# Performance work log

Measured on AMD Instinct MI355X. Metric: run time of the kernel, lower is better.

Reference implementation:

```python
import jax, jax.numpy as jnp
import numpy as np

B, T, C, FFN, N_LAYER, LAYER_ID = 4, 2048, 1024, 4096, 24, 1
EPS = 1e-5


def setup_inputs() -> dict:
    key = jax.random.key(0)
    ks = jax.random.split(key, 10)
    scale = 0.02

    def w(k, shape):
        return (jax.random.normal(k, shape, jnp.float32) * scale)

    # RWKV-4 init formulas for layer_id=1, n_layer=24 (learned params, init per source)
    r01 = LAYER_ID / (N_LAYER - 1)
    r10 = 1.0 - LAYER_ID / N_LAYER
    ddd = np.arange(C, dtype=np.float64) / C
    h = np.arange(C, dtype=np.float64)
    decay = -5.0 + 8.0 * (h / (C - 1)) ** (0.7 + 1.3 * r01)
    zigzag = np.array([(i + 1) % 3 - 1 for i in range(C)], dtype=np.float64) * 0.5
    tfirst = np.log(0.3) + zigzag

    return {
        "x": jax.random.normal(ks[0], (B, T, C), jnp.float32),
        "ln1_w": jnp.ones((C,), jnp.float32), "ln1_b": jnp.zeros((C,), jnp.float32),
        "ln2_w": jnp.ones((C,), jnp.float32), "ln2_b": jnp.zeros((C,), jnp.float32),
        "time_decay": jnp.asarray(decay, jnp.float32),
        "time_first": jnp.asarray(tfirst, jnp.float32),
        "tmk": jnp.asarray(ddd ** r10, jnp.float32),
        "tmv": jnp.asarray(ddd ** r10 + 0.3 * r01, jnp.float32),
        "tmr": jnp.asarray(ddd ** (0.5 * r10), jnp.float32),
        "att_kw": w(ks[1], (C, C)), "att_vw": w(ks[2], (C, C)),
        "att_rw": w(ks[3], (C, C)), "att_ow": w(ks[4], (C, C)),
        "f_tmk": jnp.asarray(ddd ** r10, jnp.float32),
        "f_tmr": jnp.asarray(ddd ** r10, jnp.float32),
        "f_kw": w(ks[5], (FFN, C)), "f_rw": w(ks[6], (C, C)), "f_vw": w(ks[7], (C, FFN)),
    }


def _ln(z, g, b):
    m = jnp.mean(z, axis=-1, keepdims=True)
    v = jnp.mean(jnp.square(z - m), axis=-1, keepdims=True)
    return (z - m) * jax.lax.rsqrt(v + EPS) * g + b


def _shift(z):  # token shift: prepend zero row along T, drop last
    return jnp.pad(z, ((0, 0), (1, 0), (0, 0)))[:, :-1]


def _wkv(time_decay, u, k, v):
    # Numerically-stable RWKV-4 WKV recurrence (log-space max trick).
    # k, v: [B, T, C]; time_decay, u: [C]
    w = -jnp.exp(time_decay)  # per-channel decay (negative)
    kt = jnp.moveaxis(k, 1, 0)  # [T, B, C]
    vt = jnp.moveaxis(v, 1, 0)
    aa = jnp.zeros_like(kt[0])
    bb = jnp.zeros_like(kt[0])
    pp = jnp.full_like(kt[0], -1e38)

    def step(carry, kv):
        aa, bb, pp = carry
        kk, vv = kv
        ww = u + kk
        p = jnp.maximum(pp, ww)
        e1 = jnp.exp(pp - p)
        e2 = jnp.exp(ww - p)
        out = (e1 * aa + e2 * vv) / (e1 * bb + e2)
        ww2 = pp + w
        p2 = jnp.maximum(ww2, kk)
        e1b = jnp.exp(ww2 - p2)
        e2b = jnp.exp(kk - p2)
        return (e1b * aa + e2b * vv, e1b * bb + e2b, p2), out

    _, out = jax.lax.scan(step, (aa, bb, pp), (kt, vt))
    return jnp.moveaxis(out, 0, 1)  # [B, T, C]


def reference(x, ln1_w, ln1_b, ln2_w, ln2_b, time_decay, time_first,
              tmk, tmv, tmr, att_kw, att_vw, att_rw, att_ow,
              f_tmk, f_tmr, f_kw, f_rw, f_vw):
    # --- RWKV_TimeMix (layer_id != 0; protectors are identity in fwd for finite vals) ---
    h = _ln(x, ln1_w, ln1_b)
    hx = _shift(h)
    xk = h * tmk + hx * (1.0 - tmk)
    xv = h * tmv + hx * (1.0 - tmv)
    xr = h * tmr + hx * (1.0 - tmr)
    k = jnp.einsum('btc,dc->btd', xk, att_kw)
    v = jnp.einsum('btc,dc->btd', xv, att_vw)
    sr = jax.nn.sigmoid(jnp.einsum('btc,dc->btd', xr, att_rw))
    rwkv = sr * _wkv(time_decay, time_first, k, v)
    x = x + jnp.einsum('btd,cd->btc', rwkv, att_ow)
    # --- RWKV_ChannelMix ---
    h = _ln(x, ln2_w, ln2_b)
    hx = _shift(h)
    xk = h * f_tmk + hx * (1.0 - f_tmk)
    xr = h * f_tmr + hx * (1.0 - f_tmr)
    kk = jnp.square(jax.nn.relu(jnp.einsum('btc,fc->btf', xk, f_kw)))
    kv = jnp.einsum('btf,cf->btc', kk, f_vw)
    x = x + jax.nn.sigmoid(jnp.einsum('btc,dc->btd', xr, f_rw)) * kv
    return x
```

## Files before the change

kernel.cpp:

```cpp
#include <hip/hip_runtime.h>
#include <cstdint>

#define C_DIM 1024
#define T_DIM 2048
#define B_DIM 4
#define FFN_DIM 4096
#define NROWS (B_DIM * T_DIM)
#define NELEM ((size_t)NROWS * C_DIM)
#define MB ((size_t)1 << 20)
#define NSEG 32
#define SEGL (T_DIM / NSEG)

typedef __bf16 bf16;
typedef __bf16 bf16x4 __attribute__((ext_vector_type(4)));
typedef __bf16 bf16x8 __attribute__((ext_vector_type(8)));
typedef float  floatx4 __attribute__((ext_vector_type(4)));

#define GLDS(g, l) __builtin_amdgcn_global_load_lds(                          \
    (const __attribute__((address_space(1))) void*)(g),                       \
    (__attribute__((address_space(3))) void*)(l), 16, 0, 0)

struct W7 {
    const float* s[7];
    bf16*        d[7];
    int          cum[8];
};

__global__ __launch_bounds__(256) void f2b7_kernel(W7 w)
{
    int id = blockIdx.x * 256 + threadIdx.x;
    int seg = 0;
#pragma unroll
    for (int j = 1; j < 7; ++j) if (id >= w.cum[j]) seg = j;
    int i = id - w.cum[seg];
    float4 v = ((const float4*)w.s[seg])[i];
    bf16x4 o = { (bf16)v.x, (bf16)v.y, (bf16)v.z, (bf16)v.w };
    ((bf16x4*)w.d[seg])[i] = o;
}

template<bool HASV>
__global__ __launch_bounds__(256) void lnmix_kernel(const float* __restrict__ x,
                                                    const float* __restrict__ g,
                                                    const float* __restrict__ b,
                                                    const float* __restrict__ mk,
                                                    const float* __restrict__ mv,
                                                    const float* __restrict__ mr,
                                                    bf16* __restrict__ xk,
                                                    bf16* __restrict__ xv,
                                                    bf16* __restrict__ xr)
{
    int row = blockIdx.x;
    int t   = row & (T_DIM - 1);
    int tid = threadIdx.x;
    size_t i4 = (size_t)row * 256 + tid;

    float4 v  = ((const float4*)x)[i4];
    float4 vp = make_float4(0.f, 0.f, 0.f, 0.f);
    if (t != 0) vp = ((const float4*)x)[i4 - 256];

    float s   = v.x + v.y + v.z + v.w;
    float s2  = v.x * v.x + v.y * v.y + v.z * v.z + v.w * v.w;
    float sp  = vp.x + vp.y + vp.z + vp.w;
    float sp2 = vp.x * vp.x + vp.y * vp.y + vp.z * vp.z + vp.w * vp.w;
    for (int off = 32; off > 0; off >>= 1) {
        s   += __shfl_down(s,   off);
        s2  += __shfl_down(s2,  off);
        sp  += __shfl_down(sp,  off);
        sp2 += __shfl_down(sp2, off);
    }
    __shared__ float red[16];
    int lane = tid & 63, wid = tid >> 6;
    if (lane == 0) { red[wid] = s; red[4 + wid] = s2; red[8 + wid] = sp; red[12 + wid] = sp2; }
    __syncthreads();
    s   = red[0] + red[1] + red[2] + red[3];
    s2  = red[4] + red[5] + red[6] + red[7];
    sp  = red[8] + red[9] + red[10] + red[11];
    sp2 = red[12] + red[13] + red[14] + red[15];

    float mean  = s * (1.0f / C_DIM);
    float inv   = rsqrtf(s2 * (1.0f / C_DIM) - mean * mean + 1e-5f);
    float meanp = sp * (1.0f / C_DIM);
    float invp  = rsqrtf(sp2 * (1.0f / C_DIM) - meanp * meanp + 1e-5f);

    float4 gv = ((const float4*)g)[tid];
    float4 bv = ((const float4*)b)[tid];
    float4 hv, hp;
    hv.x = (v.x - mean) * inv * gv.x + bv.x;
    hv.y = (v.y - mean) * inv * gv.y + bv.y;
    hv.z = (v.z - mean) * inv * gv.z + bv.z;
    hv.w = (v.w - mean) * inv * gv.w + bv.w;
    if (t != 0) {
        hp.x = (vp.x - meanp) * invp * gv.x + bv.x;
        hp.y = (vp.y - meanp) * invp * gv.y + bv.y;
        hp.z = (vp.z - meanp) * invp * gv.z + bv.z;
        hp.w = (vp.w - meanp) * invp * gv.w + bv.w;
    } else {
        hp = make_float4(0.f, 0.f, 0.f, 0.f);
    }

    float4 m1 = ((const float4*)mk)[tid];
    bf16x4 o;
    o.x = (bf16)(hp.x + m1.x * (hv.x - hp.x));
    o.y = (bf16)(hp.y + m1.y * (hv.y - hp.y));
    o.z = (bf16)(hp.z + m1.z * (hv.z - hp.z));
    o.w = (bf16)(hp.w + m1.w * (hv.w - hp.w));
    ((bf16x4*)xk)[i4] = o;

    if (HASV) {
        float4 m2 = ((const float4*)mv)[tid];
        o.x = (bf16)(hp.x + m2.x * (hv.x - hp.x));
        o.y = (bf16)(hp.y + m2.y * (hv.y - hp.y));
        o.z = (bf16)(hp.z + m2.z * (hv.z - hp.z));
        o.w = (bf16)(hp.w + m2.w * (hv.w - hp.w));
        ((bf16x4*)xv)[i4] = o;
    }

    float4 m3 = ((const float4*)mr)[tid];
    o.x = (bf16)(hp.x + m3.x * (hv.x - hp.x));
    o.y = (bf16)(hp.y + m3.y * (hv.y - hp.y));
    o.z = (bf16)(hp.z + m3.z * (hv.z - hp.z));
    o.w = (bf16)(hp.w + m3.w * (hv.w - hp.w));
    ((bf16x4*)xr)[i4] = o;
}

#define EPI_NONE 0
#define EPI_SIG 1
#define EPI_RELU2 2
#define EPI_ADD 3
#define EPI_SCALEADD 4

struct GemmArgs {
    const bf16* A;
    const bf16* W;
    void*       Y;
    const float* X2;
    const bf16*  S;
    int N, K, epi, outBf16;
};

__global__ __launch_bounds__(512) void gemm_p(GemmArgs pr)
{
    __shared__ unsigned short As[3 * 16384];
    __shared__ unsigned short Bs[3 * 8192];

    int tid = threadIdx.x;
    int lid = blockIdx.x;
    const bf16* PA = pr.A;
    const bf16* PW = pr.W;
    void*       PY = pr.Y;
    const float* PX2 = pr.X2;
    const bf16*  PS  = pr.S;
    int N = pr.N, K = pr.K;
    int epi = pr.epi, obf = pr.outBf16;

    int ntn = N >> 7;
    int m_t, n_t;
    if (ntn == 8) {
        int xcd = lid & 7, s = lid >> 3;
        n_t = s & 7;
        m_t = (xcd << 2) | (s >> 3);
    } else {
        int sq = lid >> 3;
        n_t = (lid & 7) * 4 + (sq & 3);
        m_t = sq >> 2;
    }
    int m0 = m_t * 256, n0 = n_t * 128;

    int wv = tid >> 6;
    int ln = tid & 63;

    int srow = wv * 16 + (ln >> 2);
    int qsw  = ((ln & 3) - ((srow >> 1) & 3)) & 3;
    const bf16* Ag = PA + (size_t)(m0 + srow) * K + qsw * 8;
    const bf16* Wg = PW + (size_t)(n0 + srow) * K + qsw * 8;
    size_t rowK128 = (size_t)128 * K;

    unsigned short* AsW = As + wv * 512;
    unsigned short* BsW = Bs + wv * 512;

    int wm = (wv & 3) * 64, wn = (wv >> 2) * 64;
    int ra0 = wm + (ln & 15);
    int rb0 = wn + (ln & 15);
    int qa  = ln >> 4;
    int abase = ra0 * 32 + (((qa + ((ra0 >> 1) & 3)) & 3) * 8);
    int bbase = rb0 * 32 + (((qa + ((rb0 >> 1) & 3)) & 3) * 8);

    floatx4 acc[4][4] = {};

#define STAGE_A(kt, bi)                                                       \
    do {                                                                      \
        const bf16* _a = Ag + (size_t)(kt) * 64;                              \
        unsigned short* _d = AsW + (bi) * 16384;                              \
        GLDS(_a,                _d);                                          \
        GLDS(_a + rowK128,      _d + 4096);                                   \
        GLDS(_a + 32,           _d + 8192);                                   \
        GLDS(_a + rowK128 + 32, _d + 12288);                                  \
    } while (0)
#define STAGE_B(kt, bi)                                                       \
    do {                                                                      \
        const bf16* _b = Wg + (size_t)(kt) * 64;                              \
        unsigned short* _d = BsW + (bi) * 8192;                               \
        GLDS(_b,      _d);                                                    \
        GLDS(_b + 32, _d + 4096);                                             \
    } while (0)

#define MFMA16(a, b)                                                          \
    do {                                                                      \
        _Pragma("unroll")                                                     \
        for (int i = 0; i < 4; ++i)                                           \
            _Pragma("unroll")                                                 \
            for (int j = 0; j < 4; ++j)                                       \
                acc[i][j] = __builtin_amdgcn_mfma_f32_16x16x32_bf16(          \
                    a[i], b[j], acc[i][j], 0, 0, 0);                          \
    } while (0)

    int nt = K >> 6;

    STAGE_A(0, 0); STAGE_B(0, 0);
    STAGE_A(1, 1); STAGE_B(1, 1);

    int bi = 0, bi2 = 2;
    for (int t = 0; t < nt; ++t) {
        if (t < nt - 1) asm volatile("s_waitcnt vmcnt(6)" ::: "memory");
        else            asm volatile("s_waitcnt vmcnt(0)" ::: "memory");
        __builtin_amdgcn_s_barrier();
        __builtin_amdgcn_sched_barrier(0);

        const unsigned short* A0 = As + bi * 16384 + abase;
        const unsigned short* B0 = Bs + bi * 8192  + bbase;
        int dost = (t + 2 < nt);

        bf16x8 a[4], b[4];
#pragma unroll
        for (int i = 0; i < 4; ++i) a[i] = *(const bf16x8*)(A0 + i * 512);
#pragma unroll
        for (int j = 0; j < 4; ++j) b[j] = *(const bf16x8*)(B0 + j * 512);
        if (dost) STAGE_A(t + 2, bi2);
        asm volatile("s_waitcnt lgkmcnt(0)" ::: "memory");
        __builtin_amdgcn_sched_barrier(0);
        MFMA16(a, b);

#pragma unroll
        for (int i = 0; i < 4; ++i) a[i] = *(const bf16x8*)(A0 + 8192 + i * 512);
#pragma unroll
        for (int j = 0; j < 4; ++j) b[j] = *(const bf16x8*)(B0 + 4096 + j * 512);
        if (dost) STAGE_B(t + 2, bi2);
        asm volatile("s_waitcnt lgkmcnt(0)" ::: "memory");
        __builtin_amdgcn_sched_barrier(0);
        MFMA16(a, b);

        bi  = (bi  == 2) ? 0 : bi  + 1;
        bi2 = (bi2 == 2) ? 0 : bi2 + 1;
    }

#undef STAGE_A
#undef STAGE_B
#undef MFMA16

    int row0 = (ln >> 4) * 4;
    int colb = n0 + wn + (ln & 15);
#pragma unroll
    for (int i = 0; i < 4; ++i) {
        int gm = m0 + wm + i * 16 + row0;
#pragma unroll
        for (int j = 0; j < 4; ++j) {
            int gn = colb + j * 16;
#pragma unroll
            for (int r = 0; r < 4; ++r) {
                size_t idx = (size_t)(gm + r) * N + gn;
                float v = acc[i][j][r];
                if (epi == EPI_SIG)        v = 1.0f / (1.0f + __expf(-v));
                else if (epi == EPI_RELU2) { float t2 = fmaxf(v, 0.0f); v = t2 * t2; }
                else if (epi == EPI_ADD)   v = PX2[idx] + v;
                else if (epi == EPI_SCALEADD) v = PX2[idx] + (float)PS[idx] * v;
                if (obf) ((bf16*)PY)[idx] = (bf16)v;
                else     ((float*)PY)[idx] = v;
            }
        }
    }
}

__global__ __launch_bounds__(512) void gemm_w(GemmArgs pr)
{
    __shared__ unsigned short As[2 * 16384];
    __shared__ unsigned short Bs[2 * 16384];

    int tid = threadIdx.x;
    int lid = blockIdx.x;
    const bf16* PA = pr.A;
    const bf16* PW = pr.W;
    void*       PY = pr.Y;
    int N = pr.N, K = pr.K;
    int epi = pr.epi, obf = pr.outBf16;

    int sq  = lid >> 3;
    int n_t = (lid & 7) * 2 + (sq & 1);
    int m_t = sq >> 1;
    int m0 = m_t * 256, n0 = n_t * 256;

    int wv = tid >> 6;
    int ln = tid & 63;

    int srow = wv * 16 + (ln >> 2);
    int qsw  = ((ln & 3) - ((srow >> 1) & 3)) & 3;
    const bf16* Ag = PA + (size_t)(m0 + srow) * K + qsw * 8;
    const bf16* Wg = PW + (size_t)(n0 + srow) * K + qsw * 8;
    size_t rowK128 = (size_t)128 * K;

    unsigned short* AsW = As + wv * 512;
    unsigned short* BsW = Bs + wv * 512;

    int wm = (wv >> 2) * 128, wn = (wv & 3) * 64;
    int ra0 = wm + (ln & 15);
    int rb0 = wn + (ln & 15);
    int qa  = ln >> 4;
    int abase = ra0 * 32 + (((qa + ((ra0 >> 1) & 3)) & 3) * 8);
    int bbase = rb0 * 32 + (((qa + ((rb0 >> 1) & 3)) & 3) * 8);

    floatx4 acc[8][4] = {};

#define WSTAGE(kt, bi)                                                        \
    do {                                                                      \
        const bf16* _a = Ag + (size_t)(kt) * 64;                              \
        const bf16* _b = Wg + (size_t)(kt) * 64;                              \
        unsigned short* _dA = AsW + (bi) * 16384;                             \
        unsigned short* _dB = BsW + (bi) * 16384;                             \
        GLDS(_a,                _dA);                 \
        GLDS(_a + rowK128,      _dA + 4096);          \
        GLDS(_a + 32,           _dA + 8192);          \
        GLDS(_a + rowK128 + 32, _dA + 12288);         \
        GLDS(_b,                _dB);                                         \
        GLDS(_b + rowK128,      _dB + 4096);                                  \
        GLDS(_b + 32,           _dB + 8192);                                  \
        GLDS(_b + rowK128 + 32, _dB + 12288);                                 \
    } while (0)

    int nt = K >> 6;

    WSTAGE(0, 0);
    asm volatile("s_waitcnt vmcnt(0)" ::: "memory");
    __builtin_amdgcn_s_barrier();
    __builtin_amdgcn_sched_barrier(0);

    for (int t = 0; t < nt; ++t) {
        int bi = t & 1;
        if (t + 1 < nt) WSTAGE(t + 1, bi ^ 1);

        const unsigned short* A0 = As + bi * 16384 + abase;
        const unsigned short* B0 = Bs + bi * 16384 + bbase;

#pragma unroll
        for (int s = 0; s < 2; ++s) {
            bf16x8 a[8], b[4];
#pragma unroll
            for (int i = 0; i < 8; ++i) a[i] = *(const bf16x8*)(A0 + s * 8192 + i * 512);
#pragma unroll
            for (int j = 0; j < 4; ++j) b[j] = *(const bf16x8*)(B0 + s * 8192 + j * 512);
            asm volatile("s_waitcnt lgkmcnt(0)" ::: "memory");
            __builtin_amdgcn_sched_barrier(0);
#pragma unroll
            for (int i = 0; i < 8; ++i)
#pragma unroll
                for (int j = 0; j < 4; ++j)
                    acc[i][j] = __builtin_amdgcn_mfma_f32_16x16x32_bf16(
                        a[i], b[j], acc[i][j], 0, 0, 0);
        }

        asm volatile("s_waitcnt vmcnt(0)" ::: "memory");
        __builtin_amdgcn_s_barrier();
        __builtin_amdgcn_sched_barrier(0);
    }
#undef WSTAGE

    int row0 = (ln >> 4) * 4;
    int colb = n0 + wn + (ln & 15);
#pragma unroll
    for (int i = 0; i < 8; ++i) {
        int gm = m0 + wm + i * 16 + row0;
#pragma unroll
        for (int j = 0; j < 4; ++j) {
            int gn = colb + j * 16;
#pragma unroll
            for (int r = 0; r < 4; ++r) {
                size_t idx = (size_t)(gm + r) * N + gn;
                float v = acc[i][j][r];
                if (epi == EPI_RELU2) { float t2 = fmaxf(v, 0.0f); v = t2 * t2; }
                else if (epi == EPI_SIG) v = 1.0f / (1.0f + __expf(-v));
                if (obf) ((bf16*)PY)[idx] = (bf16)v;
                else     ((float*)PY)[idx] = v;
            }
        }
    }
}

__global__ __launch_bounds__(256) void wkv_seg(const float* __restrict__ k,
                                               const float* __restrict__ v,
                                               const float* __restrict__ decay,
                                               float* __restrict__ sa,
                                               float* __restrict__ sb,
                                               float* __restrict__ sp)
{
    int idx = blockIdx.x * 256 + threadIdx.x;
    int c   = idx & (C_DIM - 1);
    int bs  = idx >> 10;
    int seg = bs & (NSEG - 1);
    int b   = bs >> 5;
    float w = -__expf(decay[c]);
    size_t base = ((size_t)b * T_DIM + (size_t)seg * SEGL) * C_DIM + c;
    float aa = 0.f, bb = 0.f, pp = -1e38f;
    for (int t = 0; t < SEGL; ++t) {
        size_t off = base + (size_t)t * C_DIM;
        float kk = k[off], vv = v[off];
        float ww2 = pp + w;
        float p2  = fmaxf(ww2, kk);
        float e1  = __expf(ww2 - p2);
        float e2  = __expf(kk - p2);
        aa = e1 * aa + e2 * vv;
        bb = e1 * bb + e2;
        pp = p2;
    }
    sa[idx] = aa; sb[idx] = bb; sp[idx] = pp;
}

__global__ __launch_bounds__(256) void wkv_comb(const float* __restrict__ sa,
                                                const float* __restrict__ sb,
                                                const float* __restrict__ sp,
                                                const float* __restrict__ decay,
                                                float* __restrict__ ia,
                                                float* __restrict__ ib,
                                                float* __restrict__ ip)
{
    int idx = blockIdx.x * 256 + threadIdx.x;
    int c = idx & (C_DIM - 1);
    int b = idx >> 10;
    float wL = -__expf(decay[c]) * (float)SEGL;
    float aa = 0.f, bb = 0.f, pp = -1e38f;
    size_t base = (size_t)b * NSEG * C_DIM + c;
    for (int j = 0; j < NSEG; ++j) {
        size_t o = base + (size_t)j * C_DIM;
        ia[o] = aa; ib[o] = bb; ip[o] = pp;
        float a_s = sa[o], b_s = sb[o], p_s = sp[o];
        float pd = pp + wL;
        float pn = fmaxf(pd, p_s);
        float e1 = __expf(pd - pn);
        float e2 = __expf(p_s - pn);
        aa = e1 * aa + e2 * a_s;
        bb = e1 * bb + e2 * b_s;
        pp = pn;
    }
}

__global__ __launch_bounds__(256) void wkv_out(const float* __restrict__ k,
                                               const float* __restrict__ v,
                                               const bf16* __restrict__ sr,
                                               const float* __restrict__ decay,
                                               const float* __restrict__ first,
                                               const float* __restrict__ ia,
                                               const float* __restrict__ ib,
                                               const float* __restrict__ ip,
                                               bf16* __restrict__ out)
{
    int idx = blockIdx.x * 256 + threadIdx.x;
    int c   = idx & (C_DIM - 1);
    int bs  = idx >> 10;
    int seg = bs & (NSEG - 1);
    int b   = bs >> 5;
    float w = -__expf(decay[c]);
    float u = first[c];
    float aa = ia[idx], bb = ib[idx], pp = ip[idx];
    size_t base = ((size_t)b * T_DIM + (size_t)seg * SEGL) * C_DIM + c;
    for (int t = 0; t < SEGL; ++t) {
        size_t off = base + (size_t)t * C_DIM;
        float kk = k[off], vv = v[off];
        float ww = u + kk;
        float p  = fmaxf(pp, ww);
        float e1 = __expf(pp - p);
        float e2 = __expf(ww - p);
        float o  = (e1 * aa + e2 * vv) / (e1 * bb + e2);
        out[off] = (bf16)((float)sr[off] * o);
        float ww2 = pp + w;
        float p2  = fmaxf(ww2, kk);
        float e1b = __expf(ww2 - p2);
        float e2b = __expf(kk - p2);
        aa = e1b * aa + e2b * vv;
        bb = e1b * bb + e2b;
        pp = p2;
    }
}

extern "C" void kernel_launch(void* const* d_in, const int* in_sizes, int n_in,
                              void* d_out, int out_size, void* d_ws, size_t ws_size,
                              hipStream_t stream)
{
    const float* x          = (const float*)d_in[0];
    const float* ln1_w      = (const float*)d_in[1];
    const float* ln1_b      = (const float*)d_in[2];
    const float* ln2_w      = (const float*)d_in[3];
    const float* ln2_b      = (const float*)d_in[4];
    const float* time_decay = (const float*)d_in[5];
    const float* time_first = (const float*)d_in[6];
    const float* tmk        = (const float*)d_in[7];
    const float* tmv        = (const float*)d_in[8];
    const float* tmr        = (const float*)d_in[9];
    const float* att_kw     = (const float*)d_in[10];
    const float* att_vw     = (const float*)d_in[11];
    const float* att_rw     = (const float*)d_in[12];
    const float* att_ow     = (const float*)d_in[13];
    const float* f_tmk      = (const float*)d_in[14];
    const float* f_tmr      = (const float*)d_in[15];
    const float* f_kw       = (const float*)d_in[16];
    const float* f_rw       = (const float*)d_in[17];
    const float* f_vw       = (const float*)d_in[18];
    float* out = (float*)d_out;

    char* W8 = (char*)d_ws;
    bf16* kw_b  = (bf16*)(W8 + 0 * MB);
    bf16* vw_b  = (bf16*)(W8 + 2 * MB);
    bf16* rw_b  = (bf16*)(W8 + 4 * MB);
    bf16* ow_b  = (bf16*)(W8 + 6 * MB);
    bf16* fkw_b = (bf16*)(W8 + 8 * MB);
    bf16* frw_b = (bf16*)(W8 + 16 * MB);
    bf16* fvw_b = (bf16*)(W8 + 18 * MB);

    bf16*  xk_b   = (bf16*)(W8 + 26 * MB);
    bf16*  xv_b   = (bf16*)(W8 + 42 * MB);
    bf16*  xr_b   = (bf16*)(W8 + 58 * MB);
    bf16*  rwkv_b = xk_b;
    bf16*  xk2_b  = (bf16*)(W8 + 26 * MB);
    bf16*  xr2_b  = (bf16*)(W8 + 42 * MB);
    bf16*  sr2_b  = (bf16*)(W8 + 58 * MB);
    float* kbuf   = (float*)(W8 + 74 * MB);
    float* vbuf   = (float*)(W8 + 106 * MB);
    bf16*  srb_b  = (bf16*)(W8 + 138 * MB);
    bf16*  kk_b   = (bf16*)(W8 + 106 * MB);

    size_t KB512 = (size_t)512 * 1024;
    float* sc_a = (float*)(W8 + 170 * MB);
    float* sc_b = (float*)(W8 + 170 * MB + 1 * KB512);
    float* sc_p = (float*)(W8 + 170 * MB + 2 * KB512);
    float* in_a = (float*)(W8 + 170 * MB + 3 * KB512);
    float* in_b = (float*)(W8 + 170 * MB + 4 * KB512);
    float* in_p = (float*)(W8 + 170 * MB + 5 * KB512);

    int nC4 = C_DIM * C_DIM / 4, nF4 = FFN_DIM * C_DIM / 4;
    W7 w7;
    const float* srcs[7] = { att_kw, att_vw, att_rw, att_ow, f_kw, f_rw, f_vw };
    bf16*        dsts[7] = { kw_b, vw_b, rw_b, ow_b, fkw_b, frw_b, fvw_b };
    int          cnts[7] = { nC4, nC4, nC4, nC4, nF4, nC4, nF4 };
    int cum = 0;
    for (int i = 0; i < 7; ++i) { w7.s[i] = srcs[i]; w7.d[i] = dsts[i]; w7.cum[i] = cum; cum += cnts[i]; }
    w7.cum[7] = cum;
    f2b7_kernel<<<cum / 256, 256, 0, stream>>>(w7);

    int segGrid = B_DIM * NSEG * C_DIM / 256;

    auto launch = [&](const bf16* A, const bf16* W, void* Y, const float* X2,
                      const bf16* S, int N, int K, int epi, int obf) {
        GemmArgs p; p.A = A; p.W = W; p.Y = Y; p.X2 = X2; p.S = S;
        p.N = N; p.K = K; p.epi = epi; p.outBf16 = obf;
        int grid = (NROWS / 256) * (N / 128);
        gemm_p<<<grid, 512, 0, stream>>>(p);
    };

    lnmix_kernel<true><<<NROWS, 256, 0, stream>>>(x, ln1_w, ln1_b, tmk, tmv, tmr,
                                                  xk_b, xv_b, xr_b);
    launch(xk_b, kw_b, kbuf,  nullptr, nullptr, C_DIM, C_DIM, EPI_NONE, 0);
    launch(xv_b, vw_b, vbuf,  nullptr, nullptr, C_DIM, C_DIM, EPI_NONE, 0);
    launch(xr_b, rw_b, srb_b, nullptr, nullptr, C_DIM, C_DIM, EPI_SIG,  1);
    wkv_seg<<<segGrid, 256, 0, stream>>>(kbuf, vbuf, time_decay, sc_a, sc_b, sc_p);
    wkv_comb<<<B_DIM * C_DIM / 256, 256, 0, stream>>>(sc_a, sc_b, sc_p, time_decay, in_a, in_b, in_p);
    wkv_out<<<segGrid, 256, 0, stream>>>(kbuf, vbuf, srb_b, time_decay, time_first,
                                         in_a, in_b, in_p, rwkv_b);
    launch(rwkv_b, ow_b, out, x, nullptr, C_DIM, C_DIM, EPI_ADD, 0);

    lnmix_kernel<false><<<NROWS, 256, 0, stream>>>(out, ln2_w, ln2_b, f_tmk, nullptr, f_tmr,
                                                   xk2_b, nullptr, xr2_b);
    launch(xr2_b, frw_b, sr2_b, nullptr, nullptr, C_DIM,   C_DIM, EPI_SIG,   1);
    {
        GemmArgs p; p.A = xk2_b; p.W = fkw_b; p.Y = kk_b; p.X2 = nullptr; p.S = nullptr;
        p.N = FFN_DIM; p.K = C_DIM; p.epi = EPI_RELU2; p.outBf16 = 1;
        gemm_w<<<(NROWS / 256) * (FFN_DIM / 256), 512, 0, stream>>>(p);
    }
    launch(kk_b,  fvw_b, out,   out,     sr2_b,   C_DIM, FFN_DIM, EPI_SCALEADD, 0);
}
```

Measured before the change: 528.7 us.

## Batch GEMMs into grouped launches and merge preprocessing and WKV kernels

Merges the weight fp32->bf16 conversion into the first LayerNorm/mix kernel. The three K/V/R projections now run as one grouped gemm_p launch, and the FFN key and receptance GEMMs run as one grouped gemm_w launch with a new tile mapping for N=1024. The WKV combine kernel is folded into the output kernel: each segment recomputes its prefix state from the segment summaries, which removes a launch and the intermediate state buffers. This cuts launch count and fills the GPU better with larger grids, at the cost of redundant prefix scans in the WKV output (up to 31 steps per thread) and per-block dispatch on problem index.

```diff
diff --git a/kernel.cpp b/kernel.cpp
--- a/kernel.cpp
+++ b/kernel.cpp
@@ -26,32 +26,19 @@
     int          cum[8];
 };
 
-__global__ __launch_bounds__(256) void f2b7_kernel(W7 w)
-{
-    int id = blockIdx.x * 256 + threadIdx.x;
-    int seg = 0;
-#pragma unroll
-    for (int j = 1; j < 7; ++j) if (id >= w.cum[j]) seg = j;
-    int i = id - w.cum[seg];
-    float4 v = ((const float4*)w.s[seg])[i];
-    bf16x4 o = { (bf16)v.x, (bf16)v.y, (bf16)v.z, (bf16)v.w };
-    ((bf16x4*)w.d[seg])[i] = o;
-}
-
 template<bool HASV>
-__global__ __launch_bounds__(256) void lnmix_kernel(const float* __restrict__ x,
-                                                    const float* __restrict__ g,
-                                                    const float* __restrict__ b,
-                                                    const float* __restrict__ mk,
-                                                    const float* __restrict__ mv,
-                                                    const float* __restrict__ mr,
-                                                    bf16* __restrict__ xk,
-                                                    bf16* __restrict__ xv,
-                                                    bf16* __restrict__ xr)
-{
-    int row = blockIdx.x;
-    int t   = row & (T_DIM - 1);
-    int tid = threadIdx.x;
+__device__ __forceinline__ void lnmix_body(int row, int tid,
+                                           const float* __restrict__ x,
+                                           const float* __restrict__ g,
+                                           const float* __restrict__ b,
+                                           const float* __restrict__ mk,
+                                           const float* __restrict__ mv,
+                                           const float* __restrict__ mr,
+                                           bf16* __restrict__ xk,
+                                           bf16* __restrict__ xv,
+                                           bf16* __restrict__ xr)
+{
+    int t = row & (T_DIM - 1);
     size_t i4 = (size_t)row * 256 + tid;
 
     float4 v  = ((const float4*)x)[i4];
@@ -123,6 +110,40 @@
     ((bf16x4*)xr)[i4] = o;
 }
 
+struct PreArgs {
+    W7 w;
+    const float *x, *g, *b, *mk, *mv, *mr;
+    bf16 *xk, *xv, *xr;
+};
+
+__global__ __launch_bounds__(256) void pre_kernel(PreArgs a)
+{
+    int blk = blockIdx.x, tid = threadIdx.x;
+    if (blk < NROWS) {
+        lnmix_body<true>(blk, tid, a.x, a.g, a.b, a.mk, a.mv, a.mr, a.xk, a.xv, a.xr);
+    } else {
+        int id = (blk - NROWS) * 256 + tid;
+        int seg = 0;
+#pragma unroll
+        for (int j = 1; j < 7; ++j) if (id >= a.w.cum[j]) seg = j;
+        int i = id - a.w.cum[seg];
+        float4 v = ((const float4*)a.w.s[seg])[i];
+        bf16x4 o = { (bf16)v.x, (bf16)v.y, (bf16)v.z, (bf16)v.w };
+        ((bf16x4*)a.w.d[seg])[i] = o;
+    }
+}
+
+__global__ __launch_bounds__(256) void lnmix_kernel(const float* __restrict__ x,
+                                                    const float* __restrict__ g,
+                                                    const float* __restrict__ b,
+                                                    const float* __restrict__ mk,
+                                                    const float* __restrict__ mr,
+                                                    bf16* __restrict__ xk,
+                                                    bf16* __restrict__ xr)
+{
+    lnmix_body<false>(blockIdx.x, threadIdx.x, x, g, b, mk, nullptr, mr, xk, nullptr, xr);
+}
+
 #define EPI_NONE 0
 #define EPI_SIG 1
 #define EPI_RELU2 2
@@ -137,21 +158,25 @@
     const bf16*  S;
     int N, K, epi, outBf16;
 };
-
-__global__ __launch_bounds__(512) void gemm_p(GemmArgs pr)
+struct GB3 { GemmArgs p[3]; int cum1, cum2; };
+struct GB2 { GemmArgs p[2]; int cut; };
+
+__global__ __launch_bounds__(512) void gemm_p(GB3 bt)
 {
     __shared__ unsigned short As[3 * 16384];
     __shared__ unsigned short Bs[3 * 8192];
 
     int tid = threadIdx.x;
-    int lid = blockIdx.x;
-    const bf16* PA = pr.A;
-    const bf16* PW = pr.W;
-    void*       PY = pr.Y;
-    const float* PX2 = pr.X2;
-    const bf16*  PS  = pr.S;
-    int N = pr.N, K = pr.K;
-    int epi = pr.epi, obf = pr.outBf16;
+    int id  = blockIdx.x;
+    int pi  = (id >= bt.cum1) + (id >= bt.cum2);
+    const bf16* PA = bt.p[pi].A;
+    const bf16* PW = bt.p[pi].W;
+    void*       PY = bt.p[pi].Y;
+    const float* PX2 = bt.p[pi].X2;
+    const bf16*  PS  = bt.p[pi].S;
+    int N = bt.p[pi].N, K = bt.p[pi].K;
+    int epi = bt.p[pi].epi, obf = bt.p[pi].outBf16;
+    int lid = id - (pi == 0 ? 0 : (pi == 1 ? bt.cum1 : bt.cum2));
 
     int ntn = N >> 7;
     int m_t, n_t;
@@ -280,22 +305,32 @@
     }
 }
 
-__global__ __launch_bounds__(512) void gemm_w(GemmArgs pr)
+__global__ __launch_bounds__(512) void gemm_w(GB2 bt)
 {
     __shared__ unsigned short As[2 * 16384];
     __shared__ unsigned short Bs[2 * 16384];
 
     int tid = threadIdx.x;
-    int lid = blockIdx.x;
-    const bf16* PA = pr.A;
-    const bf16* PW = pr.W;
-    void*       PY = pr.Y;
-    int N = pr.N, K = pr.K;
-    int epi = pr.epi, obf = pr.outBf16;
-
-    int sq  = lid >> 3;
-    int n_t = (lid & 7) * 2 + (sq & 1);
-    int m_t = sq >> 1;
+    int id  = blockIdx.x;
+    int pi  = (id >= bt.cut);
+    const bf16* PA = bt.p[pi].A;
+    const bf16* PW = bt.p[pi].W;
+    void*       PY = bt.p[pi].Y;
+    int N = bt.p[pi].N, K = bt.p[pi].K;
+    int epi = bt.p[pi].epi, obf = bt.p[pi].outBf16;
+    int lid = pi ? (id - bt.cut) : id;
+
+    int ntn = N >> 8;
+    int m_t, n_t;
+    if (ntn == 16) {
+        int sq = lid >> 3;
+        n_t = (lid & 7) * 2 + (sq & 1);
+        m_t = sq >> 1;
+    } else {
+        int xcd = lid & 7, s = lid >> 3;
+        n_t = s & 3;
+        m_t = (xcd << 2) | (s >> 2);
+    }
     int m0 = m_t * 256, n0 = n_t * 256;
 
     int wv = tid >> 6;
@@ -325,10 +360,10 @@
         const bf16* _b = Wg + (size_t)(kt) * 64;                              \
         unsigned short* _dA = AsW + (bi) * 16384;                             \
         unsigned short* _dB = BsW + (bi) * 16384;                             \
-        GLDS(_a,                _dA);                 \
-        GLDS(_a + rowK128,      _dA + 4096);          \
-        GLDS(_a + 32,           _dA + 8192);          \
-        GLDS(_a + rowK128 + 32, _dA + 12288);         \
+        GLDS(_a,                _dA);                                         \
+        GLDS(_a + rowK128,      _dA + 4096);                                  \
+        GLDS(_a + 32,           _dA + 8192);                                  \
+        GLDS(_a + rowK128 + 32, _dA + 12288);                                 \
         GLDS(_b,                _dB);                                         \
         GLDS(_b + rowK128,      _dB + 4096);                                  \
         GLDS(_b + 32,           _dB + 8192);                                  \
@@ -422,23 +457,29 @@
     sa[idx] = aa; sb[idx] = bb; sp[idx] = pp;
 }
 
-__global__ __launch_bounds__(256) void wkv_comb(const float* __restrict__ sa,
+__global__ __launch_bounds__(256) void wkv_out2(const float* __restrict__ k,
+                                                const float* __restrict__ v,
+                                                const bf16* __restrict__ sr,
+                                                const float* __restrict__ decay,
+                                                const float* __restrict__ first,
+                                                const float* __restrict__ sa,
                                                 const float* __restrict__ sb,
                                                 const float* __restrict__ sp,
-                                                const float* __restrict__ decay,
-                                                float* __restrict__ ia,
-                                                float* __restrict__ ib,
-                                                float* __restrict__ ip)
+                                                bf16* __restrict__ out)
 {
     int idx = blockIdx.x * 256 + threadIdx.x;
-    int c = idx & (C_DIM - 1);
-    int b = idx >> 10;
-    float wL = -__expf(decay[c]) * (float)SEGL;
+    int c   = idx & (C_DIM - 1);
+    int bs  = idx >> 10;
+    int seg = bs & (NSEG - 1);
+    int b   = bs >> 5;
+    float w = -__expf(decay[c]);
+    float u = first[c];
+
+    float wL = w * (float)SEGL;
     float aa = 0.f, bb = 0.f, pp = -1e38f;
-    size_t base = (size_t)b * NSEG * C_DIM + c;
-    for (int j = 0; j < NSEG; ++j) {
-        size_t o = base + (size_t)j * C_DIM;
-        ia[o] = aa; ib[o] = bb; ip[o] = pp;
+    size_t sbase = (size_t)b * NSEG * C_DIM + c;
+    for (int j = 0; j < seg; ++j) {
+        size_t o = sbase + (size_t)j * C_DIM;
         float a_s = sa[o], b_s = sb[o], p_s = sp[o];
         float pd = pp + wL;
         float pn = fmaxf(pd, p_s);
@@ -448,26 +489,7 @@
         bb = e1 * bb + e2 * b_s;
         pp = pn;
     }
-}
-
-__global__ __launch_bounds__(256) void wkv_out(const float* __restrict__ k,
-                                               const float* __restrict__ v,
-                                               const bf16* __restrict__ sr,
-                                               const float* __restrict__ decay,
-                                               const float* __restrict__ first,
-                                               const float* __restrict__ ia,
-                                               const float* __restrict__ ib,
-                                               const float* __restrict__ ip,
-                                               bf16* __restrict__ out)
-{
-    int idx = blockIdx.x * 256 + threadIdx.x;
-    int c   = idx & (C_DIM - 1);
-    int bs  = idx >> 10;
-    int seg = bs & (NSEG - 1);
-    int b   = bs >> 5;
-    float w = -__expf(decay[c]);
-    float u = first[c];
-    float aa = ia[idx], bb = ib[idx], pp = ip[idx];
+
     size_t base = ((size_t)b * T_DIM + (size_t)seg * SEGL) * C_DIM + c;
     for (int t = 0; t < SEGL; ++t) {
         size_t off = base + (size_t)t * C_DIM;
@@ -538,48 +560,52 @@
     float* sc_a = (float*)(W8 + 170 * MB);
     float* sc_b = (float*)(W8 + 170 * MB + 1 * KB512);
     float* sc_p = (float*)(W8 + 170 * MB + 2 * KB512);
-    float* in_a = (float*)(W8 + 170 * MB + 3 * KB512);
-    float* in_b = (float*)(W8 + 170 * MB + 4 * KB512);
-    float* in_p = (float*)(W8 + 170 * MB + 5 * KB512);
 
     int nC4 = C_DIM * C_DIM / 4, nF4 = FFN_DIM * C_DIM / 4;
-    W7 w7;
+    PreArgs pa;
     const float* srcs[7] = { att_kw, att_vw, att_rw, att_ow, f_kw, f_rw, f_vw };
     bf16*        dsts[7] = { kw_b, vw_b, rw_b, ow_b, fkw_b, frw_b, fvw_b };
     int          cnts[7] = { nC4, nC4, nC4, nC4, nF4, nC4, nF4 };
     int cum = 0;
-    for (int i = 0; i < 7; ++i) { w7.s[i] = srcs[i]; w7.d[i] = dsts[i]; w7.cum[i] = cum; cum += cnts[i]; }
-    w7.cum[7] = cum;
-    f2b7_kernel<<<cum / 256, 256, 0, stream>>>(w7);
+    for (int i = 0; i < 7; ++i) { pa.w.s[i] = srcs[i]; pa.w.d[i] = dsts[i]; pa.w.cum[i] = cum; cum += cnts[i]; }
+    pa.w.cum[7] = cum;
+    pa.x = x; pa.g = ln1_w; pa.b = ln1_b; pa.mk = tmk; pa.mv = tmv; pa.mr = tmr;
+    pa.xk = xk_b; pa.xv = xv_b; pa.xr = xr_b;
+    pre_kernel<<<NROWS + cum / 256, 256, 0, stream>>>(pa);
+
+    auto prob = [](const bf16* A, const bf16* W, void* Y, const float* X2,
+                   const bf16* S, int N, int K, int epi, int obf) {
+        GemmArgs p; p.A = A; p.W = W; p.Y = Y; p.X2 = X2; p.S = S;
+        p.N = N; p.K = K; p.epi = epi; p.outBf16 = obf; return p;
+    };
+    auto launch1 = [&](GemmArgs p, int grid) {
+        GB3 b; b.p[0] = p; b.p[1] = p; b.p[2] = p; b.cum1 = grid; b.cum2 = grid;
+        gemm_p<<<grid, 512, 0, stream>>>(b);
+    };
 
     int segGrid = B_DIM * NSEG * C_DIM / 256;
 
-    auto launch = [&](const bf16* A, const bf16* W, void* Y, const float* X2,
-                      const bf16* S, int N, int K, int epi, int obf) {
-        GemmArgs p; p.A = A; p.W = W; p.Y = Y; p.X2 = X2; p.S = S;
-        p.N = N; p.K = K; p.epi = epi; p.outBf16 = obf;
-        int grid = (NROWS / 256) * (N / 128);
-        gemm_p<<<grid, 512, 0, stream>>>(p);
-    };
-
-    lnmix_kernel<true><<<NROWS, 256, 0, stream>>>(x, ln1_w, ln1_b, tmk, tmv, tmr,
-                                                  xk_b, xv_b, xr_b);
-    launch(xk_b, kw_b, kbuf,  nullptr, nullptr, C_DIM, C_DIM, EPI_NONE, 0);
-    launch(xv_b, vw_b, vbuf,  nullptr, nullptr, C_DIM, C_DIM, EPI_NONE, 0);
-    launch(xr_b, rw_b, srb_b, nullptr, nullptr, C_DIM, C_DIM, EPI_SIG,  1);
+    {
+        GB3 b;
+        b.p[0] = prob(xk_b, kw_b, kbuf,  nullptr, nullptr, C_DIM, C_DIM, EPI_NONE, 0);
+        b.p[1] = prob(xv_b, vw_b, vbuf,  nullptr, nullptr, C_DIM, C_DIM, EPI_NONE, 0);
+        b.p[2] = prob(xr_b, rw_b, srb_b, nullptr, nullptr, C_DIM, C_DIM, EPI_SIG,  1);
+        b.cum1 = 256; b.cum2 = 512;
+        gemm_p<<<768, 512, 0, stream>>>(b);
+    }
     wkv_seg<<<segGrid, 256, 0, stream>>>(kbuf, vbuf, time_decay, sc_a, sc_b, sc_p);
-    wkv_comb<<<B_DIM * C_DIM / 256, 256, 0, stream>>>(sc_a, sc_b, sc_p, time_decay, in_a, in_b, in_p);
-    wkv_out<<<segGrid, 256, 0, stream>>>(kbuf, vbuf, srb_b, time_decay, time_first,
-                                         in_a, in_b, in_p, rwkv_b);
-    launch(rwkv_b, ow_b, out, x, nullptr, C_DIM, C_DIM, EPI_ADD, 0);
-
-    lnmix_kernel<false><<<NROWS, 256, 0, stream>>>(out, ln2_w, ln2_b, f_tmk, nullptr, f_tmr,
-                                                   xk2_b, nullptr, xr2_b);
-    launch(xr2_b, frw_b, sr2_b, nullptr, nullptr, C_DIM,   C_DIM, EPI_SIG,   1);
+    wkv_out2<<<segGrid, 256, 0, stream>>>(kbuf, vbuf, srb_b, time_decay, time_first,
+                                          sc_a, sc_b, sc_p, rwkv_b);
+    launch1(prob(rwkv_b, ow_b, out, x, nullptr, C_DIM, C_DIM, EPI_ADD, 0), 256);
+
+    lnmix_kernel<<<NROWS, 256, 0, stream>>>(out, ln2_w, ln2_b, f_tmk, f_tmr,
+                                            xk2_b, xr2_b);
     {
-        GemmArgs p; p.A = xk2_b; p.W = fkw_b; p.Y = kk_b; p.X2 = nullptr; p.S = nullptr;
-        p.N = FFN_DIM; p.K = C_DIM; p.epi = EPI_RELU2; p.outBf16 = 1;
-        gemm_w<<<(NROWS / 256) * (FFN_DIM / 256), 512, 0, stream>>>(p);
-    }
-    launch(kk_b,  fvw_b, out,   out,     sr2_b,   C_DIM, FFN_DIM, EPI_SCALEADD, 0);
-}
+        GB2 b;
+        b.p[0] = prob(xk2_b, fkw_b, kk_b,  nullptr, nullptr, FFN_DIM, C_DIM, EPI_RELU2, 1);
+        b.p[1] = prob(xr2_b, frw_b, sr2_b, nullptr, nullptr, C_DIM,   C_DIM, EPI_SIG,   1);
+        b.cut = (NROWS / 256) * (FFN_DIM / 256);
+        gemm_w<<<b.cut + (NROWS / 256) * (C_DIM / 256), 512, 0, stream>>>(b);
+    }
+    launch1(prob(kk_b, fvw_b, out, out, sr2_b, C_DIM, FFN_DIM, EPI_SCALEADD, 0), 256);
+}
```

After: 544.0 us. +2.9%, slower.

## Pipeline GEMM mainloop at half-K-tile granularity with interleaved loads and setprio

Applied to the files above, without the earlier changes.

The GEMM main loop is restructured so that LDS staging is split into four half-tile pieces (A/B by K-halves). Global-to-LDS loads are interleaved between MFMA groups, with fine-grained vmcnt waits replacing the full-tile vmcnt(0) barrier. The loop is unrolled two K-tiles at a time with an explicit epilogue. Fewer B fragments stay live, and s_setprio raises wave priority around MFMA bursts. The aim is deeper overlap of memory traffic with compute and lower register pressure, at the cost of more barriers per tile and more intricate correctness conditions on buffer reuse.

```diff
diff --git a/kernel.cpp b/kernel.cpp
--- a/kernel.cpp
+++ b/kernel.cpp
@@ -319,58 +319,83 @@
 
     floatx4 acc[8][4] = {};
 
-#define WSTAGE(kt, bi)                                                        \
+#define SA0(kt, bi) do { const bf16* _a = Ag + (size_t)(kt) * 64;             \
+        unsigned short* _d = AsW + (bi) * 16384;                              \
+        GLDS(_a, _d); GLDS(_a + rowK128, _d + 4096); } while (0)
+#define SB0(kt, bi) do { const bf16* _b = Wg + (size_t)(kt) * 64;             \
+        unsigned short* _d = BsW + (bi) * 16384;                              \
+        GLDS(_b, _d); GLDS(_b + rowK128, _d + 4096); } while (0)
+#define SA1(kt, bi) do { const bf16* _a = Ag + (size_t)(kt) * 64 + 32;        \
+        unsigned short* _d = AsW + (bi) * 16384 + 8192;                       \
+        GLDS(_a, _d); GLDS(_a + rowK128, _d + 4096); } while (0)
+#define SB1(kt, bi) do { const bf16* _b = Wg + (size_t)(kt) * 64 + 32;        \
+        unsigned short* _d = BsW + (bi) * 16384 + 8192;                       \
+        GLDS(_b, _d); GLDS(_b + rowK128, _d + 4096); } while (0)
+
+#define MROW(j, bb)                                                           \
+    acc[0][j] = __builtin_amdgcn_mfma_f32_16x16x32_bf16(a0, bb, acc[0][j], 0, 0, 0); \
+    acc[1][j] = __builtin_amdgcn_mfma_f32_16x16x32_bf16(a1, bb, acc[1][j], 0, 0, 0); \
+    acc[2][j] = __builtin_amdgcn_mfma_f32_16x16x32_bf16(a2, bb, acc[2][j], 0, 0, 0); \
+    acc[3][j] = __builtin_amdgcn_mfma_f32_16x16x32_bf16(a3, bb, acc[3][j], 0, 0, 0); \
+    acc[4][j] = __builtin_amdgcn_mfma_f32_16x16x32_bf16(a4, bb, acc[4][j], 0, 0, 0); \
+    acc[5][j] = __builtin_amdgcn_mfma_f32_16x16x32_bf16(a5, bb, acc[5][j], 0, 0, 0); \
+    acc[6][j] = __builtin_amdgcn_mfma_f32_16x16x32_bf16(a6, bb, acc[6][j], 0, 0, 0); \
+    acc[7][j] = __builtin_amdgcn_mfma_f32_16x16x32_bf16(a7, bb, acc[7][j], 0, 0, 0);
+
+#define PPAIR(VMN, bufi, ksub, STGo, STGe)                                    \
     do {                                                                      \
-        const bf16* _a = Ag + (size_t)(kt) * 64;                              \
-        const bf16* _b = Wg + (size_t)(kt) * 64;                              \
-        unsigned short* _dA = AsW + (bi) * 16384;                             \
-        unsigned short* _dB = BsW + (bi) * 16384;                             \
-        GLDS(_a,                _dA);                 \
-        GLDS(_a + rowK128,      _dA + 4096);          \
-        GLDS(_a + 32,           _dA + 8192);          \
-        GLDS(_a + rowK128 + 32, _dA + 12288);         \
-        GLDS(_b,                _dB);                                         \
-        GLDS(_b + rowK128,      _dB + 4096);                                  \
-        GLDS(_b + 32,           _dB + 8192);                                  \
-        GLDS(_b + rowK128 + 32, _dB + 12288);                                 \
+        asm volatile("s_waitcnt vmcnt(" VMN ")" ::: "memory");                \
+        __builtin_amdgcn_s_barrier();                                         \
+        __builtin_amdgcn_sched_barrier(0);                                    \
+        const unsigned short* _A = As + (bufi) * 16384 + (ksub) * 8192 + abase; \
+        const unsigned short* _B = Bs + (bufi) * 16384 + (ksub) * 8192 + bbase; \
+        bf16x8 a0, a1, a2, a3, a4, a5, a6, a7, b0, b1;                        \
+        a0 = *(const bf16x8*)(_A);        a1 = *(const bf16x8*)(_A + 512);    \
+        a2 = *(const bf16x8*)(_A + 1024); a3 = *(const bf16x8*)(_A + 1536);   \
+        a4 = *(const bf16x8*)(_A + 2048); a5 = *(const bf16x8*)(_A + 2560);   \
+        a6 = *(const bf16x8*)(_A + 3072); a7 = *(const bf16x8*)(_A + 3584);   \
+        b0 = *(const bf16x8*)(_B);        b1 = *(const bf16x8*)(_B + 512);    \
+        STGo;                                                                 \
+        asm volatile("s_waitcnt lgkmcnt(0)" ::: "memory");                    \
+        __builtin_amdgcn_sched_barrier(0);                                    \
+        __builtin_amdgcn_s_setprio(1);                                        \
+        MROW(0, b0) MROW(1, b1)                                               \
+        __builtin_amdgcn_s_setprio(0);                                        \
+        b0 = *(const bf16x8*)(_B + 1024); b1 = *(const bf16x8*)(_B + 1536);   \
+        STGe;                                                                 \
+        asm volatile("s_waitcnt lgkmcnt(0)" ::: "memory");                    \
+        __builtin_amdgcn_sched_barrier(0);                                    \
+        __builtin_amdgcn_s_setprio(1);                                        \
+        MROW(2, b0) MROW(3, b1)                                               \
+        __builtin_amdgcn_s_setprio(0);                                        \
     } while (0)
 
-    int nt = K >> 6;
-
-    WSTAGE(0, 0);
-    asm volatile("s_waitcnt vmcnt(0)" ::: "memory");
-    __builtin_amdgcn_s_barrier();
-    __builtin_amdgcn_sched_barrier(0);
-
-    for (int t = 0; t < nt; ++t) {
-        int bi = t & 1;
-        if (t + 1 < nt) WSTAGE(t + 1, bi ^ 1);
-
-        const unsigned short* A0 = As + bi * 16384 + abase;
-        const unsigned short* B0 = Bs + bi * 16384 + bbase;
-
-#pragma unroll
-        for (int s = 0; s < 2; ++s) {
-            bf16x8 a[8], b[4];
-#pragma unroll
-            for (int i = 0; i < 8; ++i) a[i] = *(const bf16x8*)(A0 + s * 8192 + i * 512);
-#pragma unroll
-            for (int j = 0; j < 4; ++j) b[j] = *(const bf16x8*)(B0 + s * 8192 + j * 512);
-            asm volatile("s_waitcnt lgkmcnt(0)" ::: "memory");
-            __builtin_amdgcn_sched_barrier(0);
-#pragma unroll
-            for (int i = 0; i < 8; ++i)
-#pragma unroll
-                for (int j = 0; j < 4; ++j)
-                    acc[i][j] = __builtin_amdgcn_mfma_f32_16x16x32_bf16(
-                        a[i], b[j], acc[i][j], 0, 0, 0);
-        }
-
-        asm volatile("s_waitcnt vmcnt(0)" ::: "memory");
-        __builtin_amdgcn_s_barrier();
-        __builtin_amdgcn_sched_barrier(0);
-    }
-#undef WSTAGE
+    int nit = K >> 7;
+
+    SA0(0, 0); SB0(0, 0); SA1(0, 0); SB1(0, 0);
+    SA0(1, 1); SB0(1, 1);
+
+    for (int j = 0; j < nit - 1; ++j) {
+        int t0 = 2 * j;
+        PPAIR("8", 0, 0, SA1(t0 + 1, 1), SB1(t0 + 1, 1));
+        PPAIR("8", 0, 1, SA0(t0 + 2, 0), SB0(t0 + 2, 0));
+        PPAIR("8", 1, 0, SA1(t0 + 2, 0), SB1(t0 + 2, 0));
+        PPAIR("8", 1, 1, SA0(t0 + 3, 1), SB0(t0 + 3, 1));
+    }
+    {
+        int t0 = 2 * (nit - 1);
+        PPAIR("8", 0, 0, SA1(t0 + 1, 1), SB1(t0 + 1, 1));
+        PPAIR("8", 0, 1, ((void)0), ((void)0));
+        PPAIR("4", 1, 0, ((void)0), ((void)0));
+        PPAIR("0", 1, 1, ((void)0), ((void)0));
+    }
+
+#undef SA0
+#undef SB0
+#undef SA1
+#undef SB1
+#undef MROW
+#undef PPAIR
 
     int row0 = (ln >> 4) * 4;
     int colb = n0 + wn + (ln & 15);
```

Result: slower. 543.7 us (+2.9%).
